# Kernel tuning notes

Measured on AMD Instinct MI355X. Metric: run time of the kernel, lower is better.

The kernel has to match this reference:

```python
import jax, jax.numpy as jnp
import numpy as np

EPS = 1e-5
MAX_DIFF = 0.01


def _conv1d(x, w, b, pad):
    # x: [B,C,L], w: [O,I,K]
    out = jax.lax.conv_general_dilated(x, w, (1,), [(pad, pad)],
                                       dimension_numbers=('NCH', 'OIH', 'NCH'))
    return out + b[None, :, None]


def _maxpool2(x):
    B, C, L = x.shape
    return x.reshape(B, C, L // 2, 2).max(-1)


def setup_inputs() -> dict:
    key = jax.random.key(0)
    ks = jax.random.split(key, 12)
    B, N, F, NF = 64, 750, 8, 250
    inp = {
        'x_sample': jax.random.normal(ks[0], (B, NF), jnp.float32),
        'x_graph': jax.random.normal(ks[1], (B, N, F), jnp.float32),
        'W1': jax.random.normal(ks[2], (NF, 250), jnp.float32) * 0.05,
        'b1': jnp.zeros((250,), jnp.float32),
        'gl': jnp.ones((250,), jnp.float32),
        'bl': jnp.zeros((250,), jnp.float32),
        'Wg': jax.random.normal(ks[3], (F, F), jnp.float32) * 0.3,
        'bg': jnp.zeros((F,), jnp.float32),
        'g1': jnp.ones((1,), jnp.float32),
        'be1': jnp.zeros((1,), jnp.float32),
        'Wc1': jax.random.normal(ks[4], (32, 1, 5), jnp.float32) * 0.3,
        'bc1': jnp.zeros((32,), jnp.float32),
        'gc1': jnp.ones((32,), jnp.float32),
        'bec1': jnp.zeros((32,), jnp.float32),
        'Wc2': jax.random.normal(ks[5], (64, 32, 5), jnp.float32) * 0.08,
        'bc2': jnp.zeros((64,), jnp.float32),
        'gc2': jnp.ones((64,), jnp.float32),
        'bec2': jnp.zeros((64,), jnp.float32),
        'Wc3': jax.random.normal(ks[6], (128, 64, 250), jnp.float32) * 0.008,
        'bc3': jnp.zeros((128,), jnp.float32),
        'Wf': jax.random.normal(ks[7], (128, 64), jnp.float32) * 0.09,
        'bf': jnp.zeros((64,), jnp.float32),
        'gf': jnp.ones((64,), jnp.float32),
        'bef': jnp.zeros((64,), jnp.float32),
        'Wo': jax.random.normal(ks[8], (64, 12), jnp.float32) * 0.12,
        'bo': jnp.zeros((12,), jnp.float32),
    }
    return inp


def reference(x_sample, x_graph, W1, b1, gl, bl, Wg, bg, g1, be1,
              Wc1, bc1, gc1, bec1, Wc2, bc2, gc2, bec2, Wc3, bc3,
              Wf, bf, gf, bef, Wo, bo):
    inv = 1.0 / jnp.sqrt(1.0 + EPS)  # eval-mode BN with mean=0, var=1
    B, N, F = x_graph.shape

    # linear1 -> BN -> ReLU (dropout is identity in eval)
    s = x_sample @ W1 + b1
    s = jax.nn.relu(s * inv * gl + bl)  # [B,250]

    # pairwise-threshold edge construction as dense masked adjacency
    d = x_graph[..., 0]  # [B,N]
    mask = (d[:, :, None] - d[:, None, :]) ** 2 < MAX_DIFF  # symmetric
    eye = jnp.eye(N, dtype=x_graph.dtype)
    A = jnp.where(mask, 1.0, 0.0) * (1.0 - eye) + eye  # + self loops (GCNConv)
    dn = jax.lax.rsqrt(A.sum(-1))  # D^{-1/2}
    An = dn[:, :, None] * A * dn[:, None, :]

    # GCNConv: D^{-1/2}(A+I)D^{-1/2} (X W) + b
    h = jnp.einsum('bij,bjf->bif', An, x_graph @ Wg) + bg
    # BatchNorm2d(1) eval (scalar affine) -> ReLU
    h = jax.nn.relu(h * inv * g1[0] + be1[0])  # [B,N,F]

    g = h.mean(-1)  # [B,N]
    x = jnp.concatenate([s, g], axis=1)[:, None, :]  # [B,1,1000]

    x = _conv1d(x, Wc1, bc1, pad=2)
    x = jax.nn.relu(x * inv * gc1[None, :, None] + bec1[None, :, None])
    x = _maxpool2(x)  # [B,32,500]

    x = _conv1d(x, Wc2, bc2, pad=2)
    x = jax.nn.relu(x * inv * gc2[None, :, None] + bec2[None, :, None])
    x = _maxpool2(x)  # [B,64,250]

    x = _conv1d(x, Wc3, bc3, pad=0)[:, :, 0]  # [B,128]

    x = x @ Wf + bf
    x = jax.nn.relu(x * inv * gf + bef)
    x = x @ Wo + bo
    return jax.nn.log_softmax(x, axis=1)
```

## Files before the change

### kernel.cpp

```cpp
#include <hip/hip_runtime.h>
#include <math.h>

#define NN 750
#define SN 1024
#define THR 0.01f

__device__ __forceinline__ float bn_inv() { return 1.0f / sqrtf(1.0f + 1e-5f); }

__global__ __launch_bounds__(256) void k_lin1(
    const float* __restrict__ xs, const float* __restrict__ W1,
    const float* __restrict__ b1, const float* __restrict__ gl,
    const float* __restrict__ bl, float* __restrict__ X0)
{
  int b = blockIdx.x, t = threadIdx.x;
  __shared__ float xsh[250];
  for (int k = t; k < 250; k += 256) xsh[k] = xs[b * 250 + k];
  __syncthreads();
  if (t < 250) {
    float acc = 0.f;
    #pragma unroll 10
    for (int k = 0; k < 250; ++k) acc = fmaf(xsh[k], W1[k * 250 + t], acc);
    float v = (acc + b1[t]) * bn_inv() * gl[t] + bl[t];
    X0[b * 1000 + t] = fmaxf(v, 0.f);
  }
}

__global__ __launch_bounds__(256) void k_graph(
    const float* __restrict__ xg, const float* __restrict__ Wg,
    const float* __restrict__ bgp, const float* __restrict__ g1p,
    const float* __restrict__ be1p, float* __restrict__ X0)
{
  int b = blockIdx.x, tid = threadIdx.x;
  __shared__ float key[SN];
  __shared__ int   idxs[SN];
  __shared__ float dns[NN];
  __shared__ unsigned short los[NN], his[NN];
  __shared__ float4 zb[2][NN * 2];
  __shared__ float wgs[64], bgs[8];

  for (int i = tid; i < SN; i += 256) {
    if (i < NN) { key[i] = xg[(b * NN + i) * 8]; idxs[i] = i; }
    else        { key[i] = 3.4e38f; idxs[i] = -1; }
  }
  if (tid < 64) wgs[tid] = Wg[tid];
  if (tid < 8)  bgs[tid] = bgp[tid];
  __syncthreads();

  for (int k = 2; k <= SN; k <<= 1) {
    for (int j = k >> 1; j > 0; j >>= 1) {
      for (int i = tid; i < SN; i += 256) {
        int ixj = i ^ j;
        if (ixj > i) {
          float a = key[i], c = key[ixj];
          bool up = ((i & k) == 0);
          if (up ? (a > c) : (a < c)) {
            key[i] = c; key[ixj] = a;
            int ta = idxs[i]; idxs[i] = idxs[ixj]; idxs[ixj] = ta;
          }
        }
      }
      __syncthreads();
    }
  }

  for (int p = tid; p < NN; p += 256) {
    float dp = key[p];
    int a = 0, bq = p;
    while (a < bq) { int m = (a + bq) >> 1; float df = dp - key[m];
      if (df * df < THR) bq = m; else a = m + 1; }
    int lo = a;
    a = p + 1; bq = NN;
    while (a < bq) { int m = (a + bq) >> 1; float df = dp - key[m];
      if (df * df < THR) a = m + 1; else bq = m; }
    int hi = a;
    los[p] = (unsigned short)lo; his[p] = (unsigned short)hi;
    dns[p] = 1.0f / sqrtf((float)(hi - lo));
  }
  __syncthreads();

  for (int p = tid; p < NN; p += 256) {
    int j = idxs[p];
    const float4* xp = (const float4*)(xg + (size_t)(b * NN + j) * 8);
    float4 x0 = xp[0], x1 = xp[1];
    float xv[8] = {x0.x, x0.y, x0.z, x0.w, x1.x, x1.y, x1.z, x1.w};
    float dn = dns[p];
    float zf[8];
    #pragma unroll
    for (int f = 0; f < 8; ++f) {
      float acc = 0.f;
      #pragma unroll
      for (int k = 0; k < 8; ++k) acc = fmaf(xv[k], wgs[k * 8 + f], acc);
      zf[f] = dn * acc;
    }
    zb[0][p * 2]     = make_float4(zf[0], zf[1], zf[2], zf[3]);
    zb[0][p * 2 + 1] = make_float4(zf[4], zf[5], zf[6], zf[7]);
  }
  __syncthreads();

  int srcb = 0;
  for (int st = 1; st < NN; st <<= 1) {
    int dstb = srcb ^ 1;
    for (int e = tid; e < NN * 2; e += 256) {
      int p = e >> 1, h = e & 1;
      float4 v = zb[srcb][e];
      if (p >= st) {
        float4 u = zb[srcb][(p - st) * 2 + h];
        v.x += u.x; v.y += u.y; v.z += u.z; v.w += u.w;
      }
      zb[dstb][e] = v;
    }
    __syncthreads();
    srcb = dstb;
  }

  float g1v = g1p[0], be1v = be1p[0], inv = bn_inv();
  for (int p = tid; p < NN; p += 256) {
    int lo = los[p], hi = his[p];
    float4 aA = zb[srcb][(hi - 1) * 2], aB = zb[srcb][(hi - 1) * 2 + 1];
    if (lo > 0) {
      float4 sA = zb[srcb][(lo - 1) * 2], sB = zb[srcb][(lo - 1) * 2 + 1];
      aA.x -= sA.x; aA.y -= sA.y; aA.z -= sA.z; aA.w -= sA.w;
      aB.x -= sB.x; aB.y -= sB.y; aB.z -= sB.z; aB.w -= sB.w;
    }
    float dn = dns[p];
    float S[8] = {aA.x, aA.y, aA.z, aA.w, aB.x, aB.y, aB.z, aB.w};
    float gsum = 0.f;
    #pragma unroll
    for (int f = 0; f < 8; ++f) {
      float h = dn * S[f] + bgs[f];
      float v = h * inv * g1v + be1v;
      gsum += fmaxf(v, 0.f);
    }
    X0[b * 1000 + 250 + idxs[p]] = gsum * 0.125f;
  }
}

__global__ __launch_bounds__(256) void k_conv1(
    const float* __restrict__ X0, const float* __restrict__ Wc1,
    const float* __restrict__ bc1, const float* __restrict__ gc1,
    const float* __restrict__ bec1, float* __restrict__ Y1)
{
  int b = blockIdx.x, p0 = blockIdx.y * 125, tid = threadIdx.x;
  __shared__ float xsh[254];
  __shared__ float w[160], bb[32], gg[32], ee[32];
  for (int i = tid; i < 254; i += 256) {
    int gq = 2 * p0 - 2 + i;
    xsh[i] = (gq >= 0 && gq < 1000) ? X0[b * 1000 + gq] : 0.f;
  }
  for (int i = tid; i < 160; i += 256) w[i] = Wc1[i];
  if (tid < 32) { bb[tid] = bc1[tid]; gg[tid] = gc1[tid]; ee[tid] = bec1[tid]; }
  __syncthreads();
  float inv = bn_inv();
  for (int o = tid; o < 32 * 125; o += 256) {
    int c = o / 125, pl = o % 125;
    int base = 2 * pl;
    float v0 = 0.f, v1 = 0.f;
    #pragma unroll
    for (int k = 0; k < 5; ++k) {
      float wk = w[c * 5 + k];
      v0 = fmaf(xsh[base + k], wk, v0);
      v1 = fmaf(xsh[base + 1 + k], wk, v1);
    }
    float s0 = fmaxf((v0 + bb[c]) * inv * gg[c] + ee[c], 0.f);
    float s1 = fmaxf((v1 + bb[c]) * inv * gg[c] + ee[c], 0.f);
    Y1[((b * 32) + c) * 500 + p0 + pl] = fmaxf(s0, s1);
  }
}

__global__ __launch_bounds__(256) void k_conv2(
    const float* __restrict__ Y1, const float* __restrict__ Wc2,
    const float* __restrict__ bc2, const float* __restrict__ gc2,
    const float* __restrict__ bec2, float* __restrict__ Y2)
{
  int b = blockIdx.x, p0 = blockIdx.y * 52, tid = threadIdx.x;
  __shared__ float xin[32][108];
  __shared__ float ws2[64 * 161];
  for (int e = tid; e < 32 * 108; e += 256) {
    int ci = e / 108, li = e % 108;
    int gq = 2 * p0 - 2 + li;
    xin[ci][li] = (gq >= 0 && gq < 500) ? Y1[((b * 32) + ci) * 500 + gq] : 0.f;
  }
  for (int e = tid; e < 64 * 160; e += 256) {
    int co = e / 160, r = e % 160;
    ws2[co * 161 + r] = Wc2[e];
  }
  __syncthreads();
  int co = tid >> 2, sub = tid & 3;
  int base = sub * 26;
  float acc[26];
  #pragma unroll
  for (int r = 0; r < 26; ++r) acc[r] = 0.f;
  for (int ci = 0; ci < 32; ++ci) {
    float xr[30];
    #pragma unroll
    for (int jj = 0; jj < 30; ++jj) xr[jj] = xin[ci][base + jj];
    #pragma unroll
    for (int k = 0; k < 5; ++k) {
      float wk = ws2[co * 161 + ci * 5 + k];
      #pragma unroll
      for (int r = 0; r < 26; ++r) acc[r] = fmaf(xr[r + k], wk, acc[r]);
    }
  }
  float inv = bn_inv();
  float bc = bc2[co], gc = gc2[co], ec = bec2[co];
  int ps = p0 + sub * 13;
  #pragma unroll
  for (int r = 0; r < 13; ++r) {
    int p = ps + r;
    if (p < 250) {
      float a0 = fmaxf((acc[2 * r] + bc) * inv * gc + ec, 0.f);
      float a1 = fmaxf((acc[2 * r + 1] + bc) * inv * gc + ec, 0.f);
      Y2[((b * 64) + co) * 250 + p] = fmaxf(a0, a1);
    }
  }
}

__global__ __launch_bounds__(256) void k_conv3(
    const float* __restrict__ Y2, const float* __restrict__ Wc3,
    float* __restrict__ C3P, int CP)
{
  int pb = blockIdx.x, tid = threadIdx.x;
  __shared__ float As[64 * 64];
  __shared__ float Bs[64 * 128];
  int bt = tid >> 5, ot = tid & 31;
  int b0 = bt * 8, o0 = ot * 4;
  float4 acc[8];
  #pragma unroll
  for (int r = 0; r < 8; ++r) acc[r] = make_float4(0.f, 0.f, 0.f, 0.f);

  for (int s = 0; s < CP; ++s) {
    int kbase = (pb * CP + s) * 64;
    __syncthreads();
    for (int e = tid; e < 4096; e += 256) {
      int bb = e >> 6, kk = e & 63;
      As[e] = Y2[bb * 16000 + kbase + kk];
    }
    for (int e = tid; e < 8192; e += 256) {
      int o = e >> 6, kk = e & 63;
      float v = Wc3[o * 16000 + kbase + kk];
      Bs[kk * 128 + ((((o >> 2) ^ (kk & 31)) << 2) | (o & 3))] = v;
    }
    __syncthreads();
    for (int ks = 0; ks < 64; ks += 4) {
      float4 av[8];
      #pragma unroll
      for (int r = 0; r < 8; ++r)
        av[r] = *(const float4*)&As[(b0 + r) * 64 + ks];
      float4 bv[4];
      #pragma unroll
      for (int q = 0; q < 4; ++q) {
        int kk = ks + q;
        bv[q] = *(const float4*)&Bs[kk * 128 + ((ot ^ (kk & 31)) << 2)];
      }
      #pragma unroll
      for (int q = 0; q < 4; ++q) {
        #pragma unroll
        for (int r = 0; r < 8; ++r) {
          float a = (q == 0) ? av[r].x : (q == 1) ? av[r].y
                  : (q == 2) ? av[r].z : av[r].w;
          acc[r].x = fmaf(a, bv[q].x, acc[r].x);
          acc[r].y = fmaf(a, bv[q].y, acc[r].y);
          acc[r].z = fmaf(a, bv[q].z, acc[r].z);
          acc[r].w = fmaf(a, bv[q].w, acc[r].w);
        }
      }
    }
  }
  #pragma unroll
  for (int r = 0; r < 8; ++r)
    *(float4*)&C3P[(size_t)pb * 8192 + (b0 + r) * 128 + o0] = acc[r];
}

__global__ __launch_bounds__(256) void k_fc(
    const float* __restrict__ C3P, const float* __restrict__ bc3,
    const float* __restrict__ Wf, const float* __restrict__ bf,
    const float* __restrict__ gf, const float* __restrict__ bef,
    const float* __restrict__ Wo, const float* __restrict__ bo,
    float* __restrict__ out, int NB)
{
  int b = blockIdx.x, t = threadIdx.x;
  __shared__ float zp[8][128];
  __shared__ float z[128];
  __shared__ float fp[4][64];
  __shared__ float f[64];

  int g = t >> 5;
  int o4 = (t & 31) * 4;
  float4 a = make_float4(0.f, 0.f, 0.f, 0.f);
  for (int c = g; c < NB; c += 8) {
    float4 v = *(const float4*)&C3P[(size_t)c * 8192 + b * 128 + o4];
    a.x += v.x; a.y += v.y; a.z += v.z; a.w += v.w;
  }
  *(float4*)&zp[g][o4] = a;
  __syncthreads();
  if (t < 128) {
    float s = bc3[t];
    #pragma unroll
    for (int gg = 0; gg < 8; ++gg) s += zp[gg][t];
    z[t] = s;
  }
  __syncthreads();

  {
    int oo = t & 63, q = t >> 6;
    float acc = 0.f;
    #pragma unroll
    for (int k = 0; k < 32; ++k) {
      int kk = q * 32 + k;
      acc = fmaf(z[kk], Wf[kk * 64 + oo], acc);
    }
    fp[q][oo] = acc;
  }
  __syncthreads();
  if (t < 64) {
    float v = fp[0][t] + fp[1][t] + fp[2][t] + fp[3][t] + bf[t];
    v = v * bn_inv() * gf[t] + bef[t];
    f[t] = fmaxf(v, 0.f);
  }
  __syncthreads();

  if (t < 64) {
    float logit = 0.f;
    if (t < 12) {
      float acc = 0.f;
      #pragma unroll 8
      for (int k = 0; k < 64; ++k) acc = fmaf(f[k], Wo[k * 12 + t], acc);
      logit = acc + bo[t];
    }
    float m = (t < 12) ? logit : -3.4e38f;
    for (int off = 32; off > 0; off >>= 1) m = fmaxf(m, __shfl_xor(m, off));
    float e = (t < 12) ? expf(logit - m) : 0.f;
    float ssum = e;
    for (int off = 32; off > 0; off >>= 1) ssum += __shfl_xor(ssum, off);
    if (t < 12) out[b * 12 + t] = logit - m - logf(ssum);
  }
}

extern "C" void kernel_launch(void* const* d_in, const int* in_sizes, int n_in,
                              void* d_out, int out_size, void* d_ws, size_t ws_size,
                              hipStream_t stream)
{
  const float* xs   = (const float*)d_in[0];
  const float* xg   = (const float*)d_in[1];
  const float* W1   = (const float*)d_in[2];
  const float* b1   = (const float*)d_in[3];
  const float* gl   = (const float*)d_in[4];
  const float* bl   = (const float*)d_in[5];
  const float* Wg   = (const float*)d_in[6];
  const float* bg   = (const float*)d_in[7];
  const float* g1   = (const float*)d_in[8];
  const float* be1  = (const float*)d_in[9];
  const float* Wc1  = (const float*)d_in[10];
  const float* bc1  = (const float*)d_in[11];
  const float* gc1  = (const float*)d_in[12];
  const float* bec1 = (const float*)d_in[13];
  const float* Wc2  = (const float*)d_in[14];
  const float* bc2  = (const float*)d_in[15];
  const float* gc2  = (const float*)d_in[16];
  const float* bec2 = (const float*)d_in[17];
  const float* Wc3  = (const float*)d_in[18];
  const float* bc3  = (const float*)d_in[19];
  const float* Wf   = (const float*)d_in[20];
  const float* bfp  = (const float*)d_in[21];
  const float* gf   = (const float*)d_in[22];
  const float* bef  = (const float*)d_in[23];
  const float* Wo   = (const float*)d_in[24];
  const float* bo   = (const float*)d_in[25];
  float* out = (float*)d_out;

  float* W   = (float*)d_ws;
  float* X0  = W;
  float* Y1  = W + 64000;
  float* Y2  = W + 1088000;
  float* C3P = W + 2112000;

  long availl = (long)(ws_size / 4) - 2112000L;
  const int cand[8] = {250, 125, 50, 25, 10, 5, 2, 1};
  int NB = 1;
  for (int i = 0; i < 8; ++i)
    if ((long)cand[i] * 8192L <= availl) { NB = cand[i]; break; }
  int CP = 250 / NB;

  k_lin1 <<<64, 256, 0, stream>>>(xs, W1, b1, gl, bl, X0);
  k_graph<<<64, 256, 0, stream>>>(xg, Wg, bg, g1, be1, X0);
  k_conv1<<<dim3(64, 4), 256, 0, stream>>>(X0, Wc1, bc1, gc1, bec1, Y1);
  k_conv2<<<dim3(64, 5), 256, 0, stream>>>(Y1, Wc2, bc2, gc2, bec2, Y2);
  k_conv3<<<NB, 256, 0, stream>>>(Y2, Wc3, C3P, CP);
  k_fc   <<<64, 256, 0, stream>>>(C3P, bc3, Wf, bfp, gf, bef, Wo, bo, out, NB);
}
```

Before: 222.5 us.

## Replace bitonic sort in GCN with rank counting and split into count/apply kernels

The single-block-per-batch GCN kernel, with its shared-memory bitonic sort and log-step prefix scan, is replaced by two kernels. The first spreads each batch over three blocks, computes each node's rank and neighbor window bounds by linear counting against encoded keys (bounds found by bisecting float thresholds), and scatters the scaled features in sorted order to global memory. The second does a warp-shuffle prefix scan and applies the windowed sums. This removes the many barrier-bound sort and scan passes and raises parallelism, at the cost of an extra launch, a global round-trip and O(N^2) compares per batch.

```diff
diff --git a/kernel.cpp b/kernel.cpp
--- a/kernel.cpp
+++ b/kernel.cpp
@@ -2,10 +2,16 @@
 #include <math.h>
 
 #define NN 750
-#define SN 1024
-#define THR 0.01f
 
 __device__ __forceinline__ float bn_inv() { return 1.0f / sqrtf(1.0f + 1e-5f); }
+
+__device__ __forceinline__ unsigned encf(float f) {
+  unsigned b = __float_as_uint(f);
+  return (b & 0x80000000u) ? ~b : (b | 0x80000000u);
+}
+__device__ __forceinline__ float decf(unsigned u) {
+  return __uint_as_float((u & 0x80000000u) ? (u & 0x7fffffffu) : ~u);
+}
 
 __global__ __launch_bounds__(256) void k_lin1(
     const float* __restrict__ xs, const float* __restrict__ W1,
@@ -25,113 +31,153 @@
   }
 }
 
-__global__ __launch_bounds__(256) void k_graph(
+__global__ __launch_bounds__(256) void k_gcn_count(
     const float* __restrict__ xg, const float* __restrict__ Wg,
+    float* __restrict__ szdn, int* __restrict__ loA, int* __restrict__ hiA,
+    float* __restrict__ dnA)
+{
+  int b = blockIdx.x, c = blockIdx.y, t = threadIdx.x;
+  __shared__ unsigned long long kL[NN];
+  __shared__ float wgs[64];
+  for (int j = t; j < NN; j += 256) {
+    float dj = xg[(size_t)(b * NN + j) * 8];
+    kL[j] = ((unsigned long long)encf(dj) << 10) | (unsigned)j;
+  }
+  if (t < 64) wgs[t] = Wg[t];
+  __syncthreads();
+  if (t >= 250) return;
+  int i = c * 250 + t;
+  float d = xg[(size_t)(b * NN + i) * 8];
+  unsigned long long ki = ((unsigned long long)encf(d) << 10) | (unsigned)i;
+
+  unsigned uf = encf(d - 0.15f);
+  unsigned ut = encf(d);
+  #pragma unroll 1
+  for (int it = 0; it < 33 && (ut - uf) > 1u; ++it) {
+    unsigned um = uf + ((ut - uf) >> 1);
+    if (d - decf(um) >= 0.1f) uf = um; else ut = um;
+  }
+  unsigned A1 = ut;
+  unsigned vf = encf(d);
+  unsigned vt = encf(d + 0.15f);
+  #pragma unroll 1
+  for (int it = 0; it < 33 && (vt - vf) > 1u; ++it) {
+    unsigned um = vf + ((vt - vf) >> 1);
+    if (d - decf(um) <= -0.1f) vt = um; else vf = um;
+  }
+  unsigned B = vt;
+
+  unsigned long long KA = (unsigned long long)A1 << 10;
+  unsigned long long KB = (unsigned long long)B << 10;
+  int rank = 0, lov = 0, hiv = 0;
+  #pragma unroll 6
+  for (int j = 0; j < NN; ++j) {
+    unsigned long long kj = kL[j];
+    rank += (kj < ki);
+    lov  += (kj < KA);
+    hiv  += (kj < KB);
+  }
+  int cnt = hiv - lov;
+  float dn = 1.0f / sqrtf((float)cnt);
+
+  const float4* xp = (const float4*)(xg + (size_t)(b * NN + i) * 8);
+  float4 x0 = xp[0], x1 = xp[1];
+  float xv[8] = {x0.x, x0.y, x0.z, x0.w, x1.x, x1.y, x1.z, x1.w};
+  float zf[8];
+  #pragma unroll
+  for (int f = 0; f < 8; ++f) {
+    float a = 0.f;
+    #pragma unroll
+    for (int k = 0; k < 8; ++k) a = fmaf(xv[k], wgs[k * 8 + f], a);
+    zf[f] = dn * a;
+  }
+  float* dst = szdn + ((size_t)b * NN + rank) * 8;
+  *(float4*)dst       = make_float4(zf[0], zf[1], zf[2], zf[3]);
+  *(float4*)(dst + 4) = make_float4(zf[4], zf[5], zf[6], zf[7]);
+  loA[b * NN + i] = lov; hiA[b * NN + i] = hiv; dnA[b * NN + i] = dn;
+}
+
+__global__ __launch_bounds__(512) void k_gcn_apply(
+    const float* __restrict__ szdn, const int* __restrict__ loA,
+    const int* __restrict__ hiA, const float* __restrict__ dnA,
     const float* __restrict__ bgp, const float* __restrict__ g1p,
     const float* __restrict__ be1p, float* __restrict__ X0)
 {
-  int b = blockIdx.x, tid = threadIdx.x;
-  __shared__ float key[SN];
-  __shared__ int   idxs[SN];
-  __shared__ float dns[NN];
-  __shared__ unsigned short los[NN], his[NN];
-  __shared__ float4 zb[2][NN * 2];
-  __shared__ float wgs[64], bgs[8];
-
-  for (int i = tid; i < SN; i += 256) {
-    if (i < NN) { key[i] = xg[(b * NN + i) * 8]; idxs[i] = i; }
-    else        { key[i] = 3.4e38f; idxs[i] = -1; }
-  }
-  if (tid < 64) wgs[tid] = Wg[tid];
-  if (tid < 8)  bgs[tid] = bgp[tid];
-  __syncthreads();
-
-  for (int k = 2; k <= SN; k <<= 1) {
-    for (int j = k >> 1; j > 0; j >>= 1) {
-      for (int i = tid; i < SN; i += 256) {
-        int ixj = i ^ j;
-        if (ixj > i) {
-          float a = key[i], c = key[ixj];
-          bool up = ((i & k) == 0);
-          if (up ? (a > c) : (a < c)) {
-            key[i] = c; key[ixj] = a;
-            int ta = idxs[i]; idxs[i] = idxs[ixj]; idxs[ixj] = ta;
-          }
-        }
+  int b = blockIdx.x, t = threadIdx.x;
+  __shared__ float P[NN * 8];
+  __shared__ float wsum[4 * 8];
+  __shared__ float bgs[8];
+  if (t < 8) bgs[t] = bgp[t];
+  for (int e = t; e < NN * 2; e += 512)
+    ((float4*)P)[e] = ((const float4*)(szdn + (size_t)b * NN * 8))[e];
+  __syncthreads();
+
+  int lane = t & 63, w = t >> 6;
+  bool scanner = (t < 256);
+  float e0[8], e01[8], s[8], sc[8];
+  if (scanner) {
+    int u = t;
+    if (u < 250) {
+      #pragma unroll
+      for (int f = 0; f < 8; ++f) e0[f] = P[(3 * u) * 8 + f];
+      #pragma unroll
+      for (int f = 0; f < 8; ++f) e01[f] = e0[f] + P[(3 * u + 1) * 8 + f];
+      #pragma unroll
+      for (int f = 0; f < 8; ++f) s[f] = e01[f] + P[(3 * u + 2) * 8 + f];
+    } else {
+      #pragma unroll
+      for (int f = 0; f < 8; ++f) { e0[f] = 0.f; e01[f] = 0.f; s[f] = 0.f; }
+    }
+    #pragma unroll
+    for (int f = 0; f < 8; ++f) sc[f] = s[f];
+    for (int dlt = 1; dlt < 64; dlt <<= 1) {
+      float o[8];
+      #pragma unroll
+      for (int f = 0; f < 8; ++f) o[f] = __shfl_up(sc[f], (unsigned)dlt, 64);
+      if (lane >= dlt) {
+        #pragma unroll
+        for (int f = 0; f < 8; ++f) sc[f] += o[f];
       }
-      __syncthreads();
-    }
-  }
-
-  for (int p = tid; p < NN; p += 256) {
-    float dp = key[p];
-    int a = 0, bq = p;
-    while (a < bq) { int m = (a + bq) >> 1; float df = dp - key[m];
-      if (df * df < THR) bq = m; else a = m + 1; }
-    int lo = a;
-    a = p + 1; bq = NN;
-    while (a < bq) { int m = (a + bq) >> 1; float df = dp - key[m];
-      if (df * df < THR) a = m + 1; else bq = m; }
-    int hi = a;
-    los[p] = (unsigned short)lo; his[p] = (unsigned short)hi;
-    dns[p] = 1.0f / sqrtf((float)(hi - lo));
-  }
-  __syncthreads();
-
-  for (int p = tid; p < NN; p += 256) {
-    int j = idxs[p];
-    const float4* xp = (const float4*)(xg + (size_t)(b * NN + j) * 8);
-    float4 x0 = xp[0], x1 = xp[1];
-    float xv[8] = {x0.x, x0.y, x0.z, x0.w, x1.x, x1.y, x1.z, x1.w};
-    float dn = dns[p];
-    float zf[8];
+    }
+    if (lane == 63) {
+      #pragma unroll
+      for (int f = 0; f < 8; ++f) wsum[w * 8 + f] = sc[f];
+    }
+  }
+  __syncthreads();
+  if (scanner && t < 250) {
+    float off[8];
+    #pragma unroll
+    for (int f = 0; f < 8; ++f) off[f] = 0.f;
+    for (int ww = 0; ww < w; ++ww) {
+      #pragma unroll
+      for (int f = 0; f < 8; ++f) off[f] += wsum[ww * 8 + f];
+    }
+    int u = t;
     #pragma unroll
     for (int f = 0; f < 8; ++f) {
-      float acc = 0.f;
-      #pragma unroll
-      for (int k = 0; k < 8; ++k) acc = fmaf(xv[k], wgs[k * 8 + f], acc);
-      zf[f] = dn * acc;
-    }
-    zb[0][p * 2]     = make_float4(zf[0], zf[1], zf[2], zf[3]);
-    zb[0][p * 2 + 1] = make_float4(zf[4], zf[5], zf[6], zf[7]);
-  }
-  __syncthreads();
-
-  int srcb = 0;
-  for (int st = 1; st < NN; st <<= 1) {
-    int dstb = srcb ^ 1;
-    for (int e = tid; e < NN * 2; e += 256) {
-      int p = e >> 1, h = e & 1;
-      float4 v = zb[srcb][e];
-      if (p >= st) {
-        float4 u = zb[srcb][(p - st) * 2 + h];
-        v.x += u.x; v.y += u.y; v.z += u.z; v.w += u.w;
-      }
-      zb[dstb][e] = v;
-    }
-    __syncthreads();
-    srcb = dstb;
-  }
-
-  float g1v = g1p[0], be1v = be1p[0], inv = bn_inv();
-  for (int p = tid; p < NN; p += 256) {
-    int lo = los[p], hi = his[p];
-    float4 aA = zb[srcb][(hi - 1) * 2], aB = zb[srcb][(hi - 1) * 2 + 1];
-    if (lo > 0) {
-      float4 sA = zb[srcb][(lo - 1) * 2], sB = zb[srcb][(lo - 1) * 2 + 1];
-      aA.x -= sA.x; aA.y -= sA.y; aA.z -= sA.z; aA.w -= sA.w;
-      aB.x -= sB.x; aB.y -= sB.y; aB.z -= sB.z; aB.w -= sB.w;
-    }
-    float dn = dns[p];
-    float S[8] = {aA.x, aA.y, aA.z, aA.w, aB.x, aB.y, aB.z, aB.w};
+      float excl = sc[f] - s[f] + off[f];
+      P[(3 * u) * 8 + f]     = excl + e0[f];
+      P[(3 * u + 1) * 8 + f] = excl + e01[f];
+      P[(3 * u + 2) * 8 + f] = excl + s[f];
+    }
+  }
+  __syncthreads();
+
+  float inv = bn_inv(), g1v = g1p[0], be1v = be1p[0];
+  for (int nn = t; nn < NN; nn += 512) {
+    int lo = loA[b * NN + nn], hi = hiA[b * NN + nn];
+    float dn = dnA[b * NN + nn];
     float gsum = 0.f;
     #pragma unroll
     for (int f = 0; f < 8; ++f) {
-      float h = dn * S[f] + bgs[f];
-      float v = h * inv * g1v + be1v;
+      float a  = P[(hi - 1) * 8 + f];
+      float bb = (lo > 0) ? P[(lo - 1) * 8 + f] : 0.f;
+      float h  = dn * (a - bb) + bgs[f];
+      float v  = h * inv * g1v + be1v;
       gsum += fmaxf(v, 0.f);
     }
-    X0[b * 1000 + 250 + idxs[p]] = gsum * 0.125f;
+    X0[b * 1000 + 250 + nn] = gsum * 0.125f;
   }
 }
 
@@ -300,7 +346,6 @@
     z[t] = s;
   }
   __syncthreads();
-
   {
     int oo = t & 63, q = t >> 6;
     float acc = 0.f;
@@ -368,23 +413,28 @@
   const float* bo   = (const float*)d_in[25];
   float* out = (float*)d_out;
 
-  float* W   = (float*)d_ws;
-  float* X0  = W;
-  float* Y1  = W + 64000;
-  float* Y2  = W + 1088000;
-  float* C3P = W + 2112000;
-
-  long availl = (long)(ws_size / 4) - 2112000L;
+  float* W    = (float*)d_ws;
+  float* X0   = W;
+  float* Y1   = W + 64000;
+  float* Y2   = W + 1088000;
+  float* szdn = W + 2112000;
+  int*   loA  = (int*)(W + 2496000);
+  int*   hiA  = (int*)(W + 2544000);
+  float* dnA  = W + 2592000;
+  float* C3P  = W + 2640000;
+
+  long availl = (long)(ws_size / 4) - 2640000L;
   const int cand[8] = {250, 125, 50, 25, 10, 5, 2, 1};
   int NB = 1;
   for (int i = 0; i < 8; ++i)
     if ((long)cand[i] * 8192L <= availl) { NB = cand[i]; break; }
   int CP = 250 / NB;
 
-  k_lin1 <<<64, 256, 0, stream>>>(xs, W1, b1, gl, bl, X0);
-  k_graph<<<64, 256, 0, stream>>>(xg, Wg, bg, g1, be1, X0);
-  k_conv1<<<dim3(64, 4), 256, 0, stream>>>(X0, Wc1, bc1, gc1, bec1, Y1);
-  k_conv2<<<dim3(64, 5), 256, 0, stream>>>(Y1, Wc2, bc2, gc2, bec2, Y2);
-  k_conv3<<<NB, 256, 0, stream>>>(Y2, Wc3, C3P, CP);
-  k_fc   <<<64, 256, 0, stream>>>(C3P, bc3, Wf, bfp, gf, bef, Wo, bo, out, NB);
-}
+  k_lin1     <<<64, 256, 0, stream>>>(xs, W1, b1, gl, bl, X0);
+  k_gcn_count<<<dim3(64, 3), 256, 0, stream>>>(xg, Wg, szdn, loA, hiA, dnA);
+  k_gcn_apply<<<64, 512, 0, stream>>>(szdn, loA, hiA, dnA, bg, g1, be1, X0);
+  k_conv1    <<<dim3(64, 4), 256, 0, stream>>>(X0, Wc1, bc1, gc1, bec1, Y1);
+  k_conv2    <<<dim3(64, 5), 256, 0, stream>>>(Y1, Wc2, bc2, gc2, bec2, Y2);
+  k_conv3    <<<NB, 256, 0, stream>>>(Y2, Wc3, C3P, CP);
+  k_fc       <<<64, 256, 0, stream>>>(C3P, bc3, Wf, bfp, gf, bef, Wo, bo, out, NB);
+}
```

Measured after the change: 200.4 us. 1.11x faster.
